# Optimization experiments

Hardware: AMD Instinct MI355X
Metric: run time of the kernel (lower is better)

Reference implementation:

```python
import jax, jax.numpy as jnp
import numpy as np

D_MODEL = 768
NUM_HEADS = 12
HEAD_DIM = D_MODEL // NUM_HEADS


def setup_inputs() -> dict:
    key = jax.random.key(0)
    ks = jax.random.split(key, 5)
    B, T = 2, 4096
    x = jax.random.normal(ks[0], (B, T, D_MODEL), dtype=jnp.float32)
    s_in = 1.0 / np.sqrt(D_MODEL)
    W_attn = jax.random.normal(ks[1], (D_MODEL, 3 * D_MODEL), dtype=jnp.float32) * s_in
    b_attn = jnp.zeros((3 * D_MODEL,), dtype=jnp.float32)
    W_proj = jax.random.normal(ks[2], (D_MODEL, D_MODEL), dtype=jnp.float32) * s_in
    b_proj = jnp.zeros((D_MODEL,), dtype=jnp.float32)
    return {"x": x, "W_attn": W_attn, "b_attn": b_attn, "W_proj": W_proj, "b_proj": b_proj}


def reference(x, W_attn, b_attn, W_proj, b_proj):
    B, T, C = x.shape
    H, D = NUM_HEADS, HEAD_DIM
    qkv = x @ W_attn + b_attn                      # [B,T,3C]
    q, k, v = jnp.split(qkv, 3, axis=-1)
    q = q.reshape(B, T, H, D).transpose(0, 2, 1, 3)  # [B,H,T,D]
    k = k.reshape(B, T, H, D).transpose(0, 2, 1, 3)
    v = v.reshape(B, T, H, D).transpose(0, 2, 1, 3)
    scores = jnp.einsum('bhqd,bhkd->bhqk', q, k) / jnp.sqrt(jnp.float32(D))
    attn = jax.nn.softmax(scores, axis=-1)          # [B,H,T,T]
    out = jnp.einsum('bhqk,bhkd->bhqd', attn, v)    # [B,H,T,D]
    out = out.transpose(0, 2, 1, 3).reshape(B, T, C)
    return out @ W_proj + b_proj
```

## Files before the change

### kernel.cpp

```cpp
#include <hip/hip_runtime.h>
#include <cstdint>
#include <cstddef>

#define DEV static __device__ __forceinline__

typedef __attribute__((ext_vector_type(8))) short bf16x8;
typedef __attribute__((ext_vector_type(4))) float f32x4;
typedef __attribute__((ext_vector_type(16))) float f32x16;

#define T_SEQ 4096
#define CDIM  768
#define NH    12
#define HD    64
#define NBH   24
#define M_ROWS 8192

#define OFF_XB   0ull
#define OFF_WAT  (OFF_XB  + (size_t)M_ROWS * CDIM * 2)
#define OFF_WPT  (OFF_WAT + (size_t)(3*CDIM) * CDIM * 2)
#define OFF_Q    (OFF_WPT + (size_t)CDIM * CDIM * 2)
#define OFF_K    (OFF_Q   + (size_t)NBH * T_SEQ * HD * 2)
#define OFF_VT   (OFF_K   + (size_t)NBH * T_SEQ * HD * 2)
#define OFF_O    (OFF_VT  + (size_t)NBH * HD * T_SEQ * 2)

DEV unsigned short f2bf(float f) {
  unsigned u = __builtin_bit_cast(unsigned, f);
  u += 0x7FFFu + ((u >> 16) & 1u);
  return (unsigned short)(u >> 16);
}

DEV void gld_lds16(const void* g, void* l) {
  __builtin_amdgcn_global_load_lds(
      (const __attribute__((address_space(1))) void*)g,
      (__attribute__((address_space(3))) void*)l, 16, 0, 0);
}

DEV void cvt8(const f32x16& s, unsigned* w) {
  asm("v_cvt_pk_bf16_f32 %0, %8, %9\n\t"
      "v_cvt_pk_bf16_f32 %1, %10, %11\n\t"
      "v_cvt_pk_bf16_f32 %2, %12, %13\n\t"
      "v_cvt_pk_bf16_f32 %3, %14, %15\n\t"
      "v_cvt_pk_bf16_f32 %4, %16, %17\n\t"
      "v_cvt_pk_bf16_f32 %5, %18, %19\n\t"
      "v_cvt_pk_bf16_f32 %6, %20, %21\n\t"
      "v_cvt_pk_bf16_f32 %7, %22, %23\n\t"
      "s_nop 3"
      : "=&v"(w[0]), "=&v"(w[1]), "=&v"(w[2]), "=&v"(w[3]),
        "=&v"(w[4]), "=&v"(w[5]), "=&v"(w[6]), "=&v"(w[7])
      : "v"(s[0]), "v"(s[1]), "v"(s[2]), "v"(s[3]),
        "v"(s[4]), "v"(s[5]), "v"(s[6]), "v"(s[7]),
        "v"(s[8]), "v"(s[9]), "v"(s[10]), "v"(s[11]),
        "v"(s[12]), "v"(s[13]), "v"(s[14]), "v"(s[15]));
}

__global__ __launch_bounds__(256) void k_conv(const float* __restrict__ in,
                                              unsigned short* __restrict__ out) {
  int i = blockIdx.x * 256 + threadIdx.x;
  const float4* p = (const float4*)in;
  float4 a = p[i * 2], b = p[i * 2 + 1];
  uint4 o;
  o.x = (unsigned)f2bf(a.x) | ((unsigned)f2bf(a.y) << 16);
  o.y = (unsigned)f2bf(a.z) | ((unsigned)f2bf(a.w) << 16);
  o.z = (unsigned)f2bf(b.x) | ((unsigned)f2bf(b.y) << 16);
  o.w = (unsigned)f2bf(b.z) | ((unsigned)f2bf(b.w) << 16);
  ((uint4*)out)[i] = o;
}

__global__ __launch_bounds__(256) void k_transpose(const float* __restrict__ in,
                                                   unsigned short* __restrict__ out,
                                                   int R, int C) {
  __shared__ float tile[64][65];
  int c0 = blockIdx.x * 64, r0 = blockIdx.y * 64;
  int tid = threadIdx.x;
  for (int i = tid; i < 4096; i += 256) {
    int r = i >> 6, c = i & 63;
    tile[r][c] = in[(size_t)(r0 + r) * C + c0 + c];
  }
  __syncthreads();
  for (int i = tid; i < 4096; i += 256) {
    int c = i >> 6, r = i & 63;
    out[(size_t)(c0 + c) * R + r0 + r] = f2bf(tile[r][c]);
  }
}

__global__ __launch_bounds__(256) void k_qkv(const unsigned short* __restrict__ A,
                                             const unsigned short* __restrict__ Bt,
                                             const float* __restrict__ bias,
                                             unsigned short* __restrict__ Qo,
                                             unsigned short* __restrict__ Ko,
                                             unsigned short* __restrict__ Vt) {
  __shared__ short As[128 * 64];
  __shared__ short Bs[128 * 64];
  const int tid = threadIdx.x;
  const int wave = tid >> 6, lane = tid & 63;
  const int wr = wave >> 1, wc = wave & 1;
  const int lin = blockIdx.y * 18 + blockIdx.x;
  const int wg = (lin & 7) * 144 + (lin >> 3);
  const int m0 = (wg / 18) * 128, n0 = (wg % 18) * 128;

  f32x4 acc[4][4] = {};

#pragma unroll 1
  for (int k0 = 0; k0 < 768; k0 += 64) {
#pragma unroll
    for (int it = 0; it < 4; ++it) {
      int chunk = wave * 4 + it;
      int slot = chunk * 64 + lane;
      int row = slot >> 3, j = slot & 7;
      int kcol = k0 + ((j ^ (row & 7)) << 3);
      gld_lds16(A  + (size_t)(m0 + row) * 768 + kcol, &As[chunk * 512]);
      gld_lds16(Bt + (size_t)(n0 + row) * 768 + kcol, &Bs[chunk * 512]);
    }
    __syncthreads();
#pragma unroll
    for (int kk = 0; kk < 2; ++kk) {
      bf16x8 af[4], bfr[4];
      int cbl = kk * 4 + (lane >> 4);
#pragma unroll
      for (int mi = 0; mi < 4; ++mi) {
        int row = wr * 64 + mi * 16 + (lane & 15);
        af[mi] = *(const bf16x8*)&As[(row * 8 + (cbl ^ (row & 7))) * 8];
      }
#pragma unroll
      for (int ni = 0; ni < 4; ++ni) {
        int row = wc * 64 + ni * 16 + (lane & 15);
        bfr[ni] = *(const bf16x8*)&Bs[(row * 8 + (cbl ^ (row & 7))) * 8];
      }
#pragma unroll
      for (int mi = 0; mi < 4; ++mi)
#pragma unroll
        for (int ni = 0; ni < 4; ++ni)
          acc[mi][ni] = __builtin_amdgcn_mfma_f32_16x16x32_bf16(af[mi], bfr[ni], acc[mi][ni], 0, 0, 0);
    }
    __syncthreads();
  }

  const int which = n0 / 768;
#pragma unroll
  for (int ni = 0; ni < 4; ++ni) {
    int col = n0 + wc * 64 + ni * 16 + (lane & 15);
    int nr = col - which * 768;
    int h = nr >> 6, d = nr & 63;
    float bi = bias[col];
#pragma unroll
    for (int mi = 0; mi < 4; ++mi) {
      int mt = m0 + wr * 64 + mi * 16 + ((lane >> 4) << 2);
      int b = mt >> 12, t = mt & 4095;
      size_t bh = (size_t)(b * NH + h);
#pragma unroll
      for (int r = 0; r < 4; ++r) {
        float v = acc[mi][ni][r] + bi;
        if (which == 0) {
          Qo[bh * (T_SEQ * HD) + (size_t)(t + r) * HD + d] = f2bf(v * 0.18033688011112042f);
        } else if (which == 1) {
          Ko[bh * (T_SEQ * HD) + (size_t)(t + r) * HD + d] = f2bf(v);
        } else {
          int tc = t + r;
          int pc = (tc & ~12) | ((tc & 4) << 1) | ((tc & 8) >> 1);
          Vt[bh * (T_SEQ * HD) + (size_t)d * T_SEQ + pc] = f2bf(v);
        }
      }
    }
  }
}

__global__ __launch_bounds__(256, 3) void k_attn(const unsigned short* __restrict__ Q,
                                                 const unsigned short* __restrict__ K,
                                                 const unsigned short* __restrict__ Vt,
                                                 unsigned short* __restrict__ O) {
  __shared__ char ldsb[2][16384];
  const int tid = threadIdx.x, wave = tid >> 6, lane = tid & 63;
  const int hi = lane >> 5, l31 = lane & 31;
  const int lin = blockIdx.y * 32 + blockIdx.x;
  const int wg = (lin & 7) * 96 + (lin >> 3);
  const int qt = wg & 31, bh = wg >> 5;
  const int b = bh / NH, h = bh % NH;
  const size_t base = (size_t)bh * T_SEQ * HD;
  const int q0 = qt * 128 + wave * 32;

  bf16x8 aq[4];
#pragma unroll
  for (int t = 0; t < 4; ++t)
    aq[t] = *(const bf16x8*)&Q[base + (size_t)(q0 + l31) * HD + t * 16 + hi * 8];

  int koff[4];
#pragma unroll
  for (int t = 0; t < 4; ++t)
    koff[t] = l31 * 128 + ((((t << 1) | hi) ^ (l31 & 7)) << 4);
  int voff[2][2];
#pragma unroll
  for (int kb = 0; kb < 2; ++kb)
#pragma unroll
    for (int ks = 0; ks < 2; ++ks)
      voff[kb][ks] = ((((kb << 2) | (ks << 1) | hi) ^ (l31 & 7)) << 4) + l31 * 128;

  f32x16 oacc0 = {}, oacc1 = {};
  float l = 0.f;

  auto STAGE = [&](int bufi, int k0) {
#pragma unroll
    for (int it = 0; it < 2; ++it) {
      int chunk = wave * 2 + it;
      int slot = chunk * 64 + lane;
      int row = slot >> 3, j = slot & 7;
      int ce = ((j ^ (row & 7)) << 3);
      gld_lds16(K  + base + (size_t)(k0 + row) * HD + ce, ldsb[bufi] + chunk * 1024);
      gld_lds16(Vt + base + (size_t)row * T_SEQ + k0 + ce, ldsb[bufi] + 8192 + chunk * 1024);
    }
  };

  STAGE(0, 0);
  __syncthreads();

  int buf = 0;
#pragma unroll 1
  for (int kt = 0; kt < 64; ++kt) {
    if (kt < 63) STAGE(buf ^ 1, (kt + 1) * 64);
    const char* Lp = ldsb[buf];
    const char* Vp = Lp + 8192;

    f32x16 s0 = {};
#pragma unroll
    for (int t = 0; t < 4; ++t) {
      bf16x8 kf = *(const bf16x8*)(Lp + koff[t]);
      s0 = __builtin_amdgcn_mfma_f32_32x32x16_bf16(kf, aq[t], s0, 0, 0, 0);
    }
#pragma unroll
    for (int r = 0; r < 16; ++r) s0[r] = __builtin_amdgcn_exp2f(s0[r]);
    {
      float a8[8];
#pragma unroll
      for (int i = 0; i < 8; ++i) a8[i] = s0[2 * i] + s0[2 * i + 1];
      float a4a = a8[0] + a8[1], a4b = a8[2] + a8[3], a4c = a8[4] + a8[5], a4d = a8[6] + a8[7];
      l += (a4a + a4b) + (a4c + a4d);
    }
    unsigned w0[8];
    cvt8(s0, w0);
    union { unsigned u[4]; bf16x8 v; } pf00, pf01;
    pf00.u[0] = w0[0]; pf00.u[1] = w0[1]; pf00.u[2] = w0[2]; pf00.u[3] = w0[3];
    pf01.u[0] = w0[4]; pf01.u[1] = w0[5]; pf01.u[2] = w0[6]; pf01.u[3] = w0[7];

    f32x16 s1 = {};
#pragma unroll
    for (int t = 0; t < 4; ++t) {
      bf16x8 kf = *(const bf16x8*)(Lp + 4096 + koff[t]);
      s1 = __builtin_amdgcn_mfma_f32_32x32x16_bf16(kf, aq[t], s1, 0, 0, 0);
    }

    {
      bf16x8 v0 = *(const bf16x8*)(Vp + voff[0][0]);
      bf16x8 v1 = *(const bf16x8*)(Vp + voff[0][1]);
      bf16x8 u0 = *(const bf16x8*)(Vp + 4096 + voff[0][0]);
      bf16x8 u1 = *(const bf16x8*)(Vp + 4096 + voff[0][1]);
      oacc0 = __builtin_amdgcn_mfma_f32_32x32x16_bf16(pf00.v, v0, oacc0, 0, 0, 0);
      oacc0 = __builtin_amdgcn_mfma_f32_32x32x16_bf16(pf01.v, v1, oacc0, 0, 0, 0);
      oacc1 = __builtin_amdgcn_mfma_f32_32x32x16_bf16(pf00.v, u0, oacc1, 0, 0, 0);
      oacc1 = __builtin_amdgcn_mfma_f32_32x32x16_bf16(pf01.v, u1, oacc1, 0, 0, 0);
    }

#pragma unroll
    for (int r = 0; r < 16; ++r) s1[r] = __builtin_amdgcn_exp2f(s1[r]);
    {
      float a8[8];
#pragma unroll
      for (int i = 0; i < 8; ++i) a8[i] = s1[2 * i] + s1[2 * i + 1];
      float a4a = a8[0] + a8[1], a4b = a8[2] + a8[3], a4c = a8[4] + a8[5], a4d = a8[6] + a8[7];
      l += (a4a + a4b) + (a4c + a4d);
    }
    unsigned w1[8];
    cvt8(s1, w1);
    union { unsigned u[4]; bf16x8 v; } pf10, pf11;
    pf10.u[0] = w1[0]; pf10.u[1] = w1[1]; pf10.u[2] = w1[2]; pf10.u[3] = w1[3];
    pf11.u[0] = w1[4]; pf11.u[1] = w1[5]; pf11.u[2] = w1[6]; pf11.u[3] = w1[7];

    {
      bf16x8 v0 = *(const bf16x8*)(Vp + voff[1][0]);
      bf16x8 v1 = *(const bf16x8*)(Vp + voff[1][1]);
      bf16x8 u0 = *(const bf16x8*)(Vp + 4096 + voff[1][0]);
      bf16x8 u1 = *(const bf16x8*)(Vp + 4096 + voff[1][1]);
      oacc0 = __builtin_amdgcn_mfma_f32_32x32x16_bf16(pf10.v, v0, oacc0, 0, 0, 0);
      oacc0 = __builtin_amdgcn_mfma_f32_32x32x16_bf16(pf11.v, v1, oacc0, 0, 0, 0);
      oacc1 = __builtin_amdgcn_mfma_f32_32x32x16_bf16(pf10.v, u0, oacc1, 0, 0, 0);
      oacc1 = __builtin_amdgcn_mfma_f32_32x32x16_bf16(pf11.v, u1, oacc1, 0, 0, 0);
    }

    __syncthreads();
    buf ^= 1;
  }

  l += __shfl_xor(l, 32, 64);

#pragma unroll
  for (int r = 0; r < 16; ++r) {
    float lt = __shfl(l, ((r & 3) + 8 * (r >> 2)) + 4 * hi, 64);
    float inv = 1.0f / lt;
    int t = q0 + ((r & 3) + 8 * (r >> 2)) + 4 * hi;
    size_t rowb = (size_t)(b * T_SEQ + t) * CDIM + h * 64;
    O[rowb + l31]      = f2bf(oacc0[r] * inv);
    O[rowb + 32 + l31] = f2bf(oacc1[r] * inv);
  }
}

__global__ __launch_bounds__(256) void k_proj(const unsigned short* __restrict__ A,
                                              const unsigned short* __restrict__ Bt,
                                              const float* __restrict__ bias,
                                              float* __restrict__ out) {
  __shared__ short As[128 * 64];
  __shared__ short Bs[128 * 64];
  const int tid = threadIdx.x;
  const int wave = tid >> 6, lane = tid & 63;
  const int wr = wave >> 1, wc = wave & 1;
  const int lin = blockIdx.y * 6 + blockIdx.x;
  const int wg = (lin & 7) * 48 + (lin >> 3);
  const int m0 = (wg / 6) * 128, n0 = (wg % 6) * 128;

  f32x4 acc[4][4] = {};

#pragma unroll 1
  for (int k0 = 0; k0 < 768; k0 += 64) {
#pragma unroll
    for (int it = 0; it < 4; ++it) {
      int chunk = wave * 4 + it;
      int slot = chunk * 64 + lane;
      int row = slot >> 3, j = slot & 7;
      int kcol = k0 + ((j ^ (row & 7)) << 3);
      gld_lds16(A  + (size_t)(m0 + row) * 768 + kcol, &As[chunk * 512]);
      gld_lds16(Bt + (size_t)(n0 + row) * 768 + kcol, &Bs[chunk * 512]);
    }
    __syncthreads();
#pragma unroll
    for (int kk = 0; kk < 2; ++kk) {
      bf16x8 af[4], bfr[4];
      int cbl = kk * 4 + (lane >> 4);
#pragma unroll
      for (int mi = 0; mi < 4; ++mi) {
        int row = wr * 64 + mi * 16 + (lane & 15);
        af[mi] = *(const bf16x8*)&As[(row * 8 + (cbl ^ (row & 7))) * 8];
      }
#pragma unroll
      for (int ni = 0; ni < 4; ++ni) {
        int row = wc * 64 + ni * 16 + (lane & 15);
        bfr[ni] = *(const bf16x8*)&Bs[(row * 8 + (cbl ^ (row & 7))) * 8];
      }
#pragma unroll
      for (int mi = 0; mi < 4; ++mi)
#pragma unroll
        for (int ni = 0; ni < 4; ++ni)
          acc[mi][ni] = __builtin_amdgcn_mfma_f32_16x16x32_bf16(af[mi], bfr[ni], acc[mi][ni], 0, 0, 0);
    }
    __syncthreads();
  }

#pragma unroll
  for (int ni = 0; ni < 4; ++ni) {
    int col = n0 + wc * 64 + ni * 16 + (lane & 15);
    float bi = bias[col];
#pragma unroll
    for (int mi = 0; mi < 4; ++mi) {
      int mt = m0 + wr * 64 + mi * 16 + ((lane >> 4) << 2);
#pragma unroll
      for (int r = 0; r < 4; ++r)
        out[(size_t)(mt + r) * CDIM + col] = acc[mi][ni][r] + bi;
    }
  }
}

extern "C" void kernel_launch(void* const* d_in, const int* in_sizes, int n_in,
                              void* d_out, int out_size, void* d_ws, size_t ws_size,
                              hipStream_t stream) {
  const float* x  = (const float*)d_in[0];
  const float* Wa = (const float*)d_in[1];
  const float* ba = (const float*)d_in[2];
  const float* Wp = (const float*)d_in[3];
  const float* bp = (const float*)d_in[4];

  char* ws = (char*)d_ws;
  unsigned short* xb  = (unsigned short*)(ws + OFF_XB);
  unsigned short* WaT = (unsigned short*)(ws + OFF_WAT);
  unsigned short* WpT = (unsigned short*)(ws + OFF_WPT);
  unsigned short* Qb  = (unsigned short*)(ws + OFF_Q);
  unsigned short* Kb  = (unsigned short*)(ws + OFF_K);
  unsigned short* Vtb = (unsigned short*)(ws + OFF_VT);
  unsigned short* Ob  = (unsigned short*)(ws + OFF_O);

  k_conv<<<3072, 256, 0, stream>>>(x, xb);
  k_transpose<<<dim3(36, 12), 256, 0, stream>>>(Wa, WaT, CDIM, 3 * CDIM);
  k_transpose<<<dim3(12, 12), 256, 0, stream>>>(Wp, WpT, CDIM, CDIM);
  k_qkv<<<dim3(18, 64), 256, 0, stream>>>(xb, WaT, ba, Qb, Kb, Vtb);
  k_attn<<<dim3(32, 24), 256, 0, stream>>>(Qb, Kb, Vtb, Ob);
  k_proj<<<dim3(6, 64), 256, 0, stream>>>(Ob, WpT, bp, (float*)d_out);
}
```

Measured before the change: 222.9 us.

## Use two waves per attention block, each computing 64 query rows

The attention kernel now launches 128 threads per block instead of 256. Each wave handles two 32-row query fragments, so every K and V fragment read from LDS is reused twice. Each wave also issues twice as many staging loads. The aim is to halve LDS read traffic per unit of MFMA work and cut the number of waves that synchronise at each barrier. In exchange, register pressure roughly doubles for accumulators and Q fragments, and the occupancy hint drops from 3 to 2, which may reduce latency hiding.

Result: slower. 229.7 us (+3.1%).

```diff
diff --git a/kernel.cpp b/kernel.cpp
--- a/kernel.cpp
+++ b/kernel.cpp
@@ -164,7 +164,7 @@
   }
 }
 
-__global__ __launch_bounds__(256, 3) void k_attn(const unsigned short* __restrict__ Q,
+__global__ __launch_bounds__(128, 2) void k_attn(const unsigned short* __restrict__ Q,
                                                  const unsigned short* __restrict__ K,
                                                  const unsigned short* __restrict__ Vt,
                                                  unsigned short* __restrict__ O) {
@@ -176,12 +176,14 @@
   const int qt = wg & 31, bh = wg >> 5;
   const int b = bh / NH, h = bh % NH;
   const size_t base = (size_t)bh * T_SEQ * HD;
-  const int q0 = qt * 128 + wave * 32;
-
-  bf16x8 aq[4];
-#pragma unroll
-  for (int t = 0; t < 4; ++t)
-    aq[t] = *(const bf16x8*)&Q[base + (size_t)(q0 + l31) * HD + t * 16 + hi * 8];
+  const int q0 = qt * 128 + wave * 64;
+
+  bf16x8 aq[2][4];
+#pragma unroll
+  for (int qf = 0; qf < 2; ++qf)
+#pragma unroll
+    for (int t = 0; t < 4; ++t)
+      aq[qf][t] = *(const bf16x8*)&Q[base + (size_t)(q0 + qf * 32 + l31) * HD + t * 16 + hi * 8];
 
   int koff[4];
 #pragma unroll
@@ -194,13 +196,13 @@
     for (int ks = 0; ks < 2; ++ks)
       voff[kb][ks] = ((((kb << 2) | (ks << 1) | hi) ^ (l31 & 7)) << 4) + l31 * 128;
 
-  f32x16 oacc0 = {}, oacc1 = {};
-  float l = 0.f;
+  f32x16 oacc[2][2] = {};
+  float lsum[2] = {0.f, 0.f};
 
   auto STAGE = [&](int bufi, int k0) {
 #pragma unroll
-    for (int it = 0; it < 2; ++it) {
-      int chunk = wave * 2 + it;
+    for (int it = 0; it < 4; ++it) {
+      int chunk = wave * 4 + it;
       int slot = chunk * 64 + lane;
       int row = slot >> 3, j = slot & 7;
       int ce = ((j ^ (row & 7)) << 3);
@@ -219,85 +221,91 @@
     const char* Lp = ldsb[buf];
     const char* Vp = Lp + 8192;
 
-    f32x16 s0 = {};
-#pragma unroll
-    for (int t = 0; t < 4; ++t) {
-      bf16x8 kf = *(const bf16x8*)(Lp + koff[t]);
-      s0 = __builtin_amdgcn_mfma_f32_32x32x16_bf16(kf, aq[t], s0, 0, 0, 0);
-    }
-#pragma unroll
-    for (int r = 0; r < 16; ++r) s0[r] = __builtin_amdgcn_exp2f(s0[r]);
-    {
-      float a8[8];
-#pragma unroll
-      for (int i = 0; i < 8; ++i) a8[i] = s0[2 * i] + s0[2 * i + 1];
-      float a4a = a8[0] + a8[1], a4b = a8[2] + a8[3], a4c = a8[4] + a8[5], a4d = a8[6] + a8[7];
-      l += (a4a + a4b) + (a4c + a4d);
-    }
-    unsigned w0[8];
-    cvt8(s0, w0);
-    union { unsigned u[4]; bf16x8 v; } pf00, pf01;
-    pf00.u[0] = w0[0]; pf00.u[1] = w0[1]; pf00.u[2] = w0[2]; pf00.u[3] = w0[3];
-    pf01.u[0] = w0[4]; pf01.u[1] = w0[5]; pf01.u[2] = w0[6]; pf01.u[3] = w0[7];
-
-    f32x16 s1 = {};
-#pragma unroll
-    for (int t = 0; t < 4; ++t) {
-      bf16x8 kf = *(const bf16x8*)(Lp + 4096 + koff[t]);
-      s1 = __builtin_amdgcn_mfma_f32_32x32x16_bf16(kf, aq[t], s1, 0, 0, 0);
-    }
-
-    {
-      bf16x8 v0 = *(const bf16x8*)(Vp + voff[0][0]);
-      bf16x8 v1 = *(const bf16x8*)(Vp + voff[0][1]);
-      bf16x8 u0 = *(const bf16x8*)(Vp + 4096 + voff[0][0]);
-      bf16x8 u1 = *(const bf16x8*)(Vp + 4096 + voff[0][1]);
-      oacc0 = __builtin_amdgcn_mfma_f32_32x32x16_bf16(pf00.v, v0, oacc0, 0, 0, 0);
-      oacc0 = __builtin_amdgcn_mfma_f32_32x32x16_bf16(pf01.v, v1, oacc0, 0, 0, 0);
-      oacc1 = __builtin_amdgcn_mfma_f32_32x32x16_bf16(pf00.v, u0, oacc1, 0, 0, 0);
-      oacc1 = __builtin_amdgcn_mfma_f32_32x32x16_bf16(pf01.v, u1, oacc1, 0, 0, 0);
-    }
-
-#pragma unroll
-    for (int r = 0; r < 16; ++r) s1[r] = __builtin_amdgcn_exp2f(s1[r]);
-    {
-      float a8[8];
-#pragma unroll
-      for (int i = 0; i < 8; ++i) a8[i] = s1[2 * i] + s1[2 * i + 1];
-      float a4a = a8[0] + a8[1], a4b = a8[2] + a8[3], a4c = a8[4] + a8[5], a4d = a8[6] + a8[7];
-      l += (a4a + a4b) + (a4c + a4d);
-    }
-    unsigned w1[8];
-    cvt8(s1, w1);
-    union { unsigned u[4]; bf16x8 v; } pf10, pf11;
-    pf10.u[0] = w1[0]; pf10.u[1] = w1[1]; pf10.u[2] = w1[2]; pf10.u[3] = w1[3];
-    pf11.u[0] = w1[4]; pf11.u[1] = w1[5]; pf11.u[2] = w1[6]; pf11.u[3] = w1[7];
-
-    {
-      bf16x8 v0 = *(const bf16x8*)(Vp + voff[1][0]);
-      bf16x8 v1 = *(const bf16x8*)(Vp + voff[1][1]);
-      bf16x8 u0 = *(const bf16x8*)(Vp + 4096 + voff[1][0]);
-      bf16x8 u1 = *(const bf16x8*)(Vp + 4096 + voff[1][1]);
-      oacc0 = __builtin_amdgcn_mfma_f32_32x32x16_bf16(pf10.v, v0, oacc0, 0, 0, 0);
-      oacc0 = __builtin_amdgcn_mfma_f32_32x32x16_bf16(pf11.v, v1, oacc0, 0, 0, 0);
-      oacc1 = __builtin_amdgcn_mfma_f32_32x32x16_bf16(pf10.v, u0, oacc1, 0, 0, 0);
-      oacc1 = __builtin_amdgcn_mfma_f32_32x32x16_bf16(pf11.v, u1, oacc1, 0, 0, 0);
+#pragma unroll
+    for (int qf = 0; qf < 2; ++qf) {
+      f32x16 s0 = {};
+#pragma unroll
+      for (int t = 0; t < 4; ++t) {
+        bf16x8 kf = *(const bf16x8*)(Lp + koff[t]);
+        s0 = __builtin_amdgcn_mfma_f32_32x32x16_bf16(kf, aq[qf][t], s0, 0, 0, 0);
+      }
+#pragma unroll
+      for (int r = 0; r < 16; ++r) s0[r] = __builtin_amdgcn_exp2f(s0[r]);
+      {
+        float a8[8];
+#pragma unroll
+        for (int i = 0; i < 8; ++i) a8[i] = s0[2 * i] + s0[2 * i + 1];
+        float a4a = a8[0] + a8[1], a4b = a8[2] + a8[3], a4c = a8[4] + a8[5], a4d = a8[6] + a8[7];
+        lsum[qf] += (a4a + a4b) + (a4c + a4d);
+      }
+      unsigned w0[8];
+      cvt8(s0, w0);
+      union { unsigned u[4]; bf16x8 v; } pf00, pf01;
+      pf00.u[0] = w0[0]; pf00.u[1] = w0[1]; pf00.u[2] = w0[2]; pf00.u[3] = w0[3];
+      pf01.u[0] = w0[4]; pf01.u[1] = w0[5]; pf01.u[2] = w0[6]; pf01.u[3] = w0[7];
+
+      f32x16 s1 = {};
+#pragma unroll
+      for (int t = 0; t < 4; ++t) {
+        bf16x8 kf = *(const bf16x8*)(Lp + 4096 + koff[t]);
+        s1 = __builtin_amdgcn_mfma_f32_32x32x16_bf16(kf, aq[qf][t], s1, 0, 0, 0);
+      }
+
+      {
+        bf16x8 v0 = *(const bf16x8*)(Vp + voff[0][0]);
+        bf16x8 v1 = *(const bf16x8*)(Vp + voff[0][1]);
+        bf16x8 u0 = *(const bf16x8*)(Vp + 4096 + voff[0][0]);
+        bf16x8 u1 = *(const bf16x8*)(Vp + 4096 + voff[0][1]);
+        oacc[qf][0] = __builtin_amdgcn_mfma_f32_32x32x16_bf16(pf00.v, v0, oacc[qf][0], 0, 0, 0);
+        oacc[qf][0] = __builtin_amdgcn_mfma_f32_32x32x16_bf16(pf01.v, v1, oacc[qf][0], 0, 0, 0);
+        oacc[qf][1] = __builtin_amdgcn_mfma_f32_32x32x16_bf16(pf00.v, u0, oacc[qf][1], 0, 0, 0);
+        oacc[qf][1] = __builtin_amdgcn_mfma_f32_32x32x16_bf16(pf01.v, u1, oacc[qf][1], 0, 0, 0);
+      }
+
+#pragma unroll
+      for (int r = 0; r < 16; ++r) s1[r] = __builtin_amdgcn_exp2f(s1[r]);
+      {
+        float a8[8];
+#pragma unroll
+        for (int i = 0; i < 8; ++i) a8[i] = s1[2 * i] + s1[2 * i + 1];
+        float a4a = a8[0] + a8[1], a4b = a8[2] + a8[3], a4c = a8[4] + a8[5], a4d = a8[6] + a8[7];
+        lsum[qf] += (a4a + a4b) + (a4c + a4d);
+      }
+      unsigned w1[8];
+      cvt8(s1, w1);
+      union { unsigned u[4]; bf16x8 v; } pf10, pf11;
+      pf10.u[0] = w1[0]; pf10.u[1] = w1[1]; pf10.u[2] = w1[2]; pf10.u[3] = w1[3];
+      pf11.u[0] = w1[4]; pf11.u[1] = w1[5]; pf11.u[2] = w1[6]; pf11.u[3] = w1[7];
+
+      {
+        bf16x8 v0 = *(const bf16x8*)(Vp + voff[1][0]);
+        bf16x8 v1 = *(const bf16x8*)(Vp + voff[1][1]);
+        bf16x8 u0 = *(const bf16x8*)(Vp + 4096 + voff[1][0]);
+        bf16x8 u1 = *(const bf16x8*)(Vp + 4096 + voff[1][1]);
+        oacc[qf][0] = __builtin_amdgcn_mfma_f32_32x32x16_bf16(pf10.v, v0, oacc[qf][0], 0, 0, 0);
+        oacc[qf][0] = __builtin_amdgcn_mfma_f32_32x32x16_bf16(pf11.v, v1, oacc[qf][0], 0, 0, 0);
+        oacc[qf][1] = __builtin_amdgcn_mfma_f32_32x32x16_bf16(pf10.v, u0, oacc[qf][1], 0, 0, 0);
+        oacc[qf][1] = __builtin_amdgcn_mfma_f32_32x32x16_bf16(pf11.v, u1, oacc[qf][1], 0, 0, 0);
+      }
     }
 
     __syncthreads();
     buf ^= 1;
   }
 
-  l += __shfl_xor(l, 32, 64);
-
-#pragma unroll
-  for (int r = 0; r < 16; ++r) {
-    float lt = __shfl(l, ((r & 3) + 8 * (r >> 2)) + 4 * hi, 64);
-    float inv = 1.0f / lt;
-    int t = q0 + ((r & 3) + 8 * (r >> 2)) + 4 * hi;
-    size_t rowb = (size_t)(b * T_SEQ + t) * CDIM + h * 64;
-    O[rowb + l31]      = f2bf(oacc0[r] * inv);
-    O[rowb + 32 + l31] = f2bf(oacc1[r] * inv);
+#pragma unroll
+  for (int qf = 0; qf < 2; ++qf) {
+    float l = lsum[qf];
+    l += __shfl_xor(l, 32, 64);
+#pragma unroll
+    for (int r = 0; r < 16; ++r) {
+      float lt = __shfl(l, ((r & 3) + 8 * (r >> 2)) + 4 * hi, 64);
+      float inv = 1.0f / lt;
+      int t = q0 + qf * 32 + ((r & 3) + 8 * (r >> 2)) + 4 * hi;
+      size_t rowb = (size_t)(b * T_SEQ + t) * CDIM + h * 64;
+      O[rowb + l31]      = f2bf(oacc[qf][0][r] * inv);
+      O[rowb + 32 + l31] = f2bf(oacc[qf][1][r] * inv);
+    }
   }
 }
 
@@ -387,6 +395,6 @@
   k_transpose<<<dim3(36, 12), 256, 0, stream>>>(Wa, WaT, CDIM, 3 * CDIM);
   k_transpose<<<dim3(12, 12), 256, 0, stream>>>(Wp, WpT, CDIM, CDIM);
   k_qkv<<<dim3(18, 64), 256, 0, stream>>>(xb, WaT, ba, Qb, Kb, Vtb);
-  k_attn<<<dim3(32, 24), 256, 0, stream>>>(Qb, Kb, Vtb, Ob);
+  k_attn<<<dim3(32, 24), 128, 0, stream>>>(Qb, Kb, Vtb, Ob);
   k_proj<<<dim3(6, 64), 256, 0, stream>>>(Ob, WpT, bp, (float*)d_out);
 }
```
